# Kernel optimization log

Hardware: AMD Instinct MI355X
Metric: run time of the kernel (lower is better)

Reference implementation:

```python
import jax, jax.numpy as jnp
import numpy as np

N = 50000
E = 1600000
H = 64          # hidden_dim
EIN = 8         # edges_in_d (7 edge feats + 1 distance)
NORM_FACTOR = 100.0
NORM_CONSTANT = 1.0


def setup_inputs() -> dict:
    key = jax.random.key(0)
    ks = jax.random.split(key, 9)
    h = jax.random.normal(ks[0], (N, H), dtype=jnp.float32)
    coord = jax.random.normal(ks[1], (N, 3), dtype=jnp.float32)
    edge_index = jax.random.randint(ks[2], (2, E), 0, N)
    edge_attr = jax.random.normal(ks[3], (E, EIN), dtype=jnp.float32)
    # coord_mlp params: Linear(2H+EIN,H) -> SiLU -> Linear(H,H) -> SiLU -> Linear(H,1,bias=False)
    din = 2 * H + EIN
    W1 = jax.random.normal(ks[4], (din, H), dtype=jnp.float32) / np.sqrt(din)
    b1 = jnp.zeros((H,), dtype=jnp.float32)
    W2 = jax.random.normal(ks[5], (H, H), dtype=jnp.float32) / np.sqrt(H)
    b2 = jnp.zeros((H,), dtype=jnp.float32)
    # final layer xavier_uniform with gain=0.001 -> very small weights
    W3 = jax.random.uniform(ks[6], (H, 1), dtype=jnp.float32, minval=-1.0, maxval=1.0) * (0.001 * np.sqrt(6.0 / (H + 1)))
    return {"h": h, "coord": coord, "edge_index": edge_index, "edge_attr": edge_attr,
            "W1": W1, "b1": b1, "W2": W2, "b2": b2, "W3": W3}


def reference(h, coord, edge_index, edge_attr, W1, b1, W2, b2, W3):
    row, col = edge_index[0], edge_index[1]
    # coord2diff (norm_constant=1)
    coord_diff = coord[row] - coord[col]                       # [E,3]
    radial = jnp.sum(coord_diff ** 2, axis=1, keepdims=True)   # [E,1]
    norm = jnp.sqrt(radial + 1e-8)
    coord_diff = coord_diff / (norm + NORM_CONSTANT)
    # gather + concat -> edge MLP (SiLU activations), tanh=False path
    inp = jnp.concatenate([h[row], h[col], edge_attr], axis=1)  # [E, 2H+EIN]
    x1 = jax.nn.silu(inp @ W1 + b1)
    x2 = jax.nn.silu(x1 @ W2 + b2)
    scal = x2 @ W3                                              # [E,1]
    trans = coord_diff * scal                                   # [E,3]
    # unsorted_segment_sum with 'sum' aggregation -> divide by normalization_factor
    agg = jax.ops.segment_sum(trans, row, num_segments=N) / NORM_FACTOR  # [N,3]
    return coord + agg
```

## Files before the change

### kernel.cpp

```cpp
#include <hip/hip_runtime.h>
#include <math.h>

#define HD   64
#define EIN  8
#define SAS  168
#define W2S  72
#define NORM_INV 0.01f
#define NTH  256
#define NBLK 1280
#define NWAVES (NBLK * (NTH / 64))

typedef short bf16x8 __attribute__((ext_vector_type(8)));
typedef float f32x4  __attribute__((ext_vector_type(4)));
typedef float f4v    __attribute__((ext_vector_type(4)));

__device__ __forceinline__ unsigned short f2bf(float f) {
    union { float f; unsigned u; } v; v.f = f;
    unsigned r = v.u + 0x7FFFu + ((v.u >> 16) & 1u);
    return (unsigned short)(r >> 16);
}
__device__ __forceinline__ unsigned pk2(float a, float b) {
    return (unsigned)f2bf(a) | ((unsigned)f2bf(b) << 16);
}
__device__ __forceinline__ unsigned cvt_pk_bf16(float lo, float hi) {
    unsigned r;
    asm("v_cvt_pk_bf16_f32 %0, %1, %2" : "=v"(r) : "v"(lo), "v"(hi));
    return r;
}
__device__ __forceinline__ float silu_f(float x) {
    return x * __builtin_amdgcn_rcpf(1.0f + __expf(-x));
}
__device__ __forceinline__ bf16x8 pack_f8(f4v a, f4v b) {
    union { bf16x8 v; uint4 u; } pk;
    pk.u.x = pk2(a.x, a.y); pk.u.y = pk2(a.z, a.w);
    pk.u.z = pk2(b.x, b.y); pk.u.w = pk2(b.z, b.w);
    return pk.v;
}

__global__ void prep_h_kernel(const float* __restrict__ h, unsigned char* __restrict__ hf8,
                              int nq, const float* __restrict__ coord,
                              float* __restrict__ out, int n3) {
    int i = blockIdx.x * blockDim.x + threadIdx.x;
    if (i < nq) {
        f4v v = reinterpret_cast<const f4v*>(h)[i];
        int p = __builtin_amdgcn_cvt_pk_fp8_f32(v.x, v.y, 0, false);
        p     = __builtin_amdgcn_cvt_pk_fp8_f32(v.z, v.w, p, true);
        reinterpret_cast<int*>(hf8)[i] = p;
    }
    if (i < n3) out[i] = coord[i];
}

__global__ void prep_out_kernel(const float* __restrict__ coord,
                                float* __restrict__ out, int n3) {
    int i = blockIdx.x * blockDim.x + threadIdx.x;
    if (i < n3) out[i] = coord[i];
}

template <bool HB>
__global__ __launch_bounds__(NTH, 5) void egnn_mfma_kernel(
    const float* __restrict__ h,
    const unsigned char* __restrict__ hf8,
    const float* __restrict__ coord,
    const int*   __restrict__ eidx,
    const float* __restrict__ eattr,
    const float* __restrict__ W1f,
    const float* __restrict__ W2f,
    const float* __restrict__ b1,
    const float* __restrict__ b2,
    const float* __restrict__ W3,
    float* __restrict__ out,
    int E_)
{
    constexpr int LDS_BYTES = HB ? 28416 : 40704;
    __shared__ __align__(16) char lds[LDS_BYTES];

    unsigned long*  sW1f8 = (unsigned long*)lds;
    unsigned short* sW1b  = (unsigned short*)(lds + 8192);
    unsigned short* sW1   = (unsigned short*)lds;
    unsigned short* sW2   = (unsigned short*)(lds + (HB ? 9216  : 21504));
    unsigned short* sX1   = (unsigned short*)(lds + (HB ? 18432 : 30720));
    float*          sB1   = (float*)(lds + (HB ? 27648 : 39936));
    float*          sB2   = sB1 + 64;
    float*          sW3   = sB1 + 128;

    const int t = threadIdx.x;

    if (HB) {
        for (int f = t; f < 16 * 64; f += NTH) {
            int frag = f >> 6, ln = f & 63;
            int nt = frag >> 2, s = frag & 3;
            int mm = ln & 15, qq = ln >> 4;
            int n2 = nt * 16 + mm, kb = s * 32 + qq * 8;
            unsigned long v = 0;
#pragma unroll
            for (int j = 0; j < 8; j += 2) {
                float a = W1f[(kb + j) * 64 + n2] * 8.0f;
                float b = W1f[(kb + j + 1) * 64 + n2] * 8.0f;
                int p = __builtin_amdgcn_cvt_pk_fp8_f32(a, b, 0, false);
                v |= ((unsigned long)(unsigned)(p & 0xFFFF)) << (j * 8);
            }
            sW1f8[f] = v;
        }
        for (int i = t; i < 64 * 8; i += NTH) {
            int n2 = i >> 3, kk = i & 7;
            sW1b[i] = f2bf(W1f[(128 + kk) * 64 + n2]);
        }
    } else {
        for (int i = t; i < 136 * 64; i += NTH) {
            int k = i >> 6, n = i & 63;
            sW1[n * SAS + k] = f2bf(W1f[i]);
        }
        for (int i = t; i < 24 * 64; i += NTH) {
            int n = i / 24, k = 136 + (i - n * 24);
            sW1[n * SAS + k] = 0;
        }
    }
    for (int i = t; i < 64 * 64; i += NTH) {
        int k = i >> 6, n = i & 63;
        sW2[n * W2S + k] = f2bf(W2f[i]);
    }
    if (t < 64) sB1[t] = b1[t];
    else if (t < 128) sB2[t - 64] = b2[t - 64];
    else if (t < 192) sW3[t - 128] = W3[t - 128];
    __syncthreads();

    const int w = t >> 6, lane = t & 63;
    const int m = lane & 15, q = lane >> 4;

    unsigned short* x1Row = sX1 + (16 * w + m) * W2S;

    const int ngroups = (E_ + 15) >> 4;
    for (int g = blockIdx.x * (NTH / 64) + w; g < ngroups; g += NWAVES) {
        int e = g * 16 + m;
        int ec = (e < E_) ? e : (E_ - 1);
        int row = __builtin_nontemporal_load(eidx + ec);
        int col = __builtin_nontemporal_load(eidx + (size_t)E_ + ec);

        float cr = 0.f, cc = 0.f;
        if (q < 3) { cr = coord[row * 3 + q]; cc = coord[col * 3 + q]; }

        bf16x8 bf4;
        {
            union { bf16x8 v; uint4 u; } pk;
            pk.u.x = 0; pk.u.y = 0; pk.u.z = 0; pk.u.w = 0;
            if (q == 0) {
                const f4v* ea = (const f4v*)(eattr + (size_t)ec * EIN);
                f4v a0 = __builtin_nontemporal_load(ea);
                f4v a1 = __builtin_nontemporal_load(ea + 1);
                pk.u.x = cvt_pk_bf16(a0.x, a0.y);
                pk.u.y = cvt_pk_bf16(a0.z, a0.w);
                pk.u.z = cvt_pk_bf16(a1.x, a1.y);
                pk.u.w = cvt_pk_bf16(a1.z, a1.w);
            }
            bf4 = pk.v;
        }

        f32x4 acc1[4] = {};

        if (HB) {
            const unsigned long* hr8 = (const unsigned long*)(hf8 + (size_t)row * HD);
            const unsigned long* hc8 = (const unsigned long*)(hf8 + (size_t)col * HD);
            long b0 = (long)hr8[q];
            long b1v = (long)hr8[4 + q];
            long b2v = (long)hc8[q];
            long b3v = (long)hc8[4 + q];
            __builtin_amdgcn_s_setprio(1);
#define L1F8(S, B)                                                            \
            _Pragma("unroll")                                                 \
            for (int nt = 0; nt < 4; ++nt) {                                  \
                long a8 = (long)sW1f8[((nt << 2) | (S)) * 64 + lane];         \
                acc1[nt] = __builtin_amdgcn_mfma_f32_16x16x32_fp8_fp8(a8, B, acc1[nt], 0, 0, 0); \
            }
            L1F8(0, b0)
            L1F8(1, b1v)
            L1F8(2, b2v)
            L1F8(3, b3v)
#undef L1F8
#pragma unroll
            for (int nt = 0; nt < 4; ++nt) {
                bf16x8 afb = *(const bf16x8*)(sW1b + (16 * nt + m) * 8);
                acc1[nt] = __builtin_amdgcn_mfma_f32_16x16x32_bf16(afb, bf4, acc1[nt], 0, 0, 0);
            }
            __builtin_amdgcn_s_setprio(0);
        } else {
            bf16x8 bf[5];
            const f4v* hr = (const f4v*)(h + (size_t)row * HD);
            const f4v* hc = (const f4v*)(h + (size_t)col * HD);
#pragma unroll
            for (int s = 0; s < 4; ++s) {
                const f4v* src = (s < 2) ? hr : hc;
                f4v a = src[(s & 1) * 8 + q * 2];
                f4v b = src[(s & 1) * 8 + q * 2 + 1];
                bf[s] = pack_f8(a, b);
            }
            bf[4] = bf4;
#pragma unroll
            for (int s = 0; s < 5; ++s) {
#pragma unroll
                for (int nt = 0; nt < 4; ++nt) {
                    bf16x8 afrag = *(const bf16x8*)(sW1 + (16 * nt + m) * SAS + s * 32 + q * 8);
                    acc1[nt] = __builtin_amdgcn_mfma_f32_16x16x32_bf16(afrag, bf[s], acc1[nt], 0, 0, 0);
                }
            }
        }

        const float sc = HB ? 0.125f : 1.0f;
#pragma unroll
        for (int nt = 0; nt < 4; ++nt) {
            float4 bb = *(const float4*)(&sB1[16 * nt + 4 * q]);
            uint2 o;
            o.x = cvt_pk_bf16(silu_f(fmaf(acc1[nt][0], sc, bb.x)),
                              silu_f(fmaf(acc1[nt][1], sc, bb.y)));
            o.y = cvt_pk_bf16(silu_f(fmaf(acc1[nt][2], sc, bb.z)),
                              silu_f(fmaf(acc1[nt][3], sc, bb.w)));
            *((uint2*)(x1Row + 16 * nt + 4 * q)) = o;
        }

        f32x4 acc2[4] = {};
        __builtin_amdgcn_s_setprio(1);
#pragma unroll
        for (int s = 0; s < 2; ++s) {
            bf16x8 bfrag = *(const bf16x8*)(x1Row + s * 32 + q * 8);
#pragma unroll
            for (int nt = 0; nt < 4; ++nt) {
                bf16x8 afrag = *(const bf16x8*)(sW2 + (16 * nt + m) * W2S + s * 32 + q * 8);
                acc2[nt] = __builtin_amdgcn_mfma_f32_16x16x32_bf16(afrag, bfrag, acc2[nt], 0, 0, 0);
            }
        }
        __builtin_amdgcn_s_setprio(0);

        float p = 0.f;
#pragma unroll
        for (int nt = 0; nt < 4; ++nt) {
            float4 b2v2 = *(const float4*)(&sB2[16 * nt + 4 * q]);
            float4 w3v  = *(const float4*)(&sW3[16 * nt + 4 * q]);
            p = fmaf(silu_f(acc2[nt][0] + b2v2.x), w3v.x, p);
            p = fmaf(silu_f(acc2[nt][1] + b2v2.y), w3v.y, p);
            p = fmaf(silu_f(acc2[nt][2] + b2v2.z), w3v.z, p);
            p = fmaf(silu_f(acc2[nt][3] + b2v2.w), w3v.w, p);
        }
        p += __shfl_xor(p, 16);
        p += __shfl_xor(p, 32);

        float cd = cr - cc;
        float r2 = cd * cd;
        r2 += __shfl_xor(r2, 16);
        r2 += __shfl_xor(r2, 32);
        if (e < E_ && q < 3) {
            float inv = __builtin_amdgcn_rcpf(sqrtf(r2 + 1e-8f) + 1.0f);
            atomicAdd(&out[row * 3 + q], cd * (p * NORM_INV * inv));
        }
    }
}

extern "C" void kernel_launch(void* const* d_in, const int* in_sizes, int n_in,
                              void* d_out, int out_size, void* d_ws, size_t ws_size,
                              hipStream_t stream) {
    const float* h         = (const float*)d_in[0];
    const float* coord     = (const float*)d_in[1];
    const int*   eidx      = (const int*)  d_in[2];
    const float* edge_attr = (const float*)d_in[3];
    const float* W1        = (const float*)d_in[4];
    const float* b1        = (const float*)d_in[5];
    const float* W2        = (const float*)d_in[6];
    const float* b2        = (const float*)d_in[7];
    const float* W3        = (const float*)d_in[8];
    float* out = (float*)d_out;

    int E_ = in_sizes[2] / 2;
    int n3 = out_size;
    int nf = in_sizes[0];

    if (ws_size >= (size_t)nf) {
        unsigned char* hf8 = (unsigned char*)d_ws;
        int nq = nf / 4;
        int pgrid = (nq > n3 ? nq : n3);
        hipLaunchKernelGGL(prep_h_kernel, dim3((pgrid + 255) / 256), dim3(256), 0, stream,
                           h, hf8, nq, coord, out, n3);
        hipLaunchKernelGGL((egnn_mfma_kernel<true>), dim3(NBLK), dim3(NTH), 0, stream,
                           h, hf8, coord, eidx, edge_attr, W1, W2, b1, b2, W3, out, E_);
    } else {
        hipLaunchKernelGGL(prep_out_kernel, dim3((n3 + 255) / 256), dim3(256), 0, stream,
                           coord, out, n3);
        hipLaunchKernelGGL((egnn_mfma_kernel<false>), dim3(NBLK), dim3(NTH), 0, stream,
                           h, (const unsigned char*)nullptr, coord, eidx, edge_attr,
                           W1, W2, b1, b2, W3, out, E_);
    }
}
```

Baseline: 218.3 us.

## Run second MLP layer in FP8 MFMA and share reciprocal across SiLU pairs

In the HB path, W2 is prepacked into FP8 MFMA fragments scaled by 8, and x1 activations are stored as FP8 in LDS. The second layer then uses the 16x16x32 fp8 MFMA, and the scale is undone before the bias. SiLU is computed in pairs with one reciprocal per two values, and the block count rises to 1536 because the smaller LDS footprint permits more resident blocks. The aim is to cut LDS traffic and footprint, MFMA cost and transcendental count, at the price of lower precision for the hidden activations. The paired reciprocal can also overflow when the exponentials are large.

```diff
diff --git a/kernel.cpp b/kernel.cpp
--- a/kernel.cpp
+++ b/kernel.cpp
@@ -5,9 +5,10 @@
 #define EIN  8
 #define SAS  168
 #define W2S  72
+#define X1BS 72
 #define NORM_INV 0.01f
 #define NTH  256
-#define NBLK 1280
+#define NBLK 1536
 #define NWAVES (NBLK * (NTH / 64))
 
 typedef short bf16x8 __attribute__((ext_vector_type(8)));
@@ -29,6 +30,13 @@
 }
 __device__ __forceinline__ float silu_f(float x) {
     return x * __builtin_amdgcn_rcpf(1.0f + __expf(-x));
+}
+__device__ __forceinline__ void silu2(float x, float y, float& sx, float& sy) {
+    float a = 1.0f + __expf(-x);
+    float b = 1.0f + __expf(-y);
+    float r = __builtin_amdgcn_rcpf(a * b);
+    sx = x * (b * r);
+    sy = y * (a * r);
 }
 __device__ __forceinline__ bf16x8 pack_f8(f4v a, f4v b) {
     union { bf16x8 v; uint4 u; } pk;
@@ -71,15 +79,17 @@
     float* __restrict__ out,
     int E_)
 {
-    constexpr int LDS_BYTES = HB ? 28416 : 40704;
+    constexpr int LDS_BYTES = HB ? 18688 : 40704;
     __shared__ __align__(16) char lds[LDS_BYTES];
 
     unsigned long*  sW1f8 = (unsigned long*)lds;
     unsigned short* sW1b  = (unsigned short*)(lds + 8192);
+    unsigned long*  sW2f8 = (unsigned long*)(lds + 9216);
+    unsigned char*  sX1b  = (unsigned char*)(lds + 13312);
     unsigned short* sW1   = (unsigned short*)lds;
-    unsigned short* sW2   = (unsigned short*)(lds + (HB ? 9216  : 21504));
-    unsigned short* sX1   = (unsigned short*)(lds + (HB ? 18432 : 30720));
-    float*          sB1   = (float*)(lds + (HB ? 27648 : 39936));
+    unsigned short* sW2   = (unsigned short*)(lds + 21504);
+    unsigned short* sX1   = (unsigned short*)(lds + 30720);
+    float*          sB1   = (float*)(lds + (HB ? 17920 : 39936));
     float*          sB2   = sB1 + 64;
     float*          sW3   = sB1 + 128;
 
@@ -105,6 +115,21 @@
             int n2 = i >> 3, kk = i & 7;
             sW1b[i] = f2bf(W1f[(128 + kk) * 64 + n2]);
         }
+        for (int f = t; f < 8 * 64; f += NTH) {
+            int frag = f >> 6, ln = f & 63;
+            int nt = frag >> 1, s = frag & 1;
+            int mm = ln & 15, qq = ln >> 4;
+            int n2 = nt * 16 + mm, kb = s * 32 + qq * 8;
+            unsigned long v = 0;
+#pragma unroll
+            for (int j = 0; j < 8; j += 2) {
+                float a = W2f[(kb + j) * 64 + n2] * 8.0f;
+                float b = W2f[(kb + j + 1) * 64 + n2] * 8.0f;
+                int p = __builtin_amdgcn_cvt_pk_fp8_f32(a, b, 0, false);
+                v |= ((unsigned long)(unsigned)(p & 0xFFFF)) << (j * 8);
+            }
+            sW2f8[f] = v;
+        }
     } else {
         for (int i = t; i < 136 * 64; i += NTH) {
             int k = i >> 6, n = i & 63;
@@ -114,10 +139,10 @@
             int n = i / 24, k = 136 + (i - n * 24);
             sW1[n * SAS + k] = 0;
         }
-    }
-    for (int i = t; i < 64 * 64; i += NTH) {
-        int k = i >> 6, n = i & 63;
-        sW2[n * W2S + k] = f2bf(W2f[i]);
+        for (int i = t; i < 64 * 64; i += NTH) {
+            int k = i >> 6, n = i & 63;
+            sW2[n * W2S + k] = f2bf(W2f[i]);
+        }
     }
     if (t < 64) sB1[t] = b1[t];
     else if (t < 128) sB2[t - 64] = b2[t - 64];
@@ -127,7 +152,8 @@
     const int w = t >> 6, lane = t & 63;
     const int m = lane & 15, q = lane >> 4;
 
-    unsigned short* x1Row = sX1 + (16 * w + m) * W2S;
+    unsigned char*  x1RowB = sX1b + (16 * w + m) * X1BS;
+    unsigned short* x1Row  = sX1 + (16 * w + m) * W2S;
 
     const int ngroups = (E_ + 15) >> 4;
     for (int g = blockIdx.x * (NTH / 64) + w; g < ngroups; g += NWAVES) {
@@ -208,36 +234,59 @@
 #pragma unroll
         for (int nt = 0; nt < 4; ++nt) {
             float4 bb = *(const float4*)(&sB1[16 * nt + 4 * q]);
-            uint2 o;
-            o.x = cvt_pk_bf16(silu_f(fmaf(acc1[nt][0], sc, bb.x)),
-                              silu_f(fmaf(acc1[nt][1], sc, bb.y)));
-            o.y = cvt_pk_bf16(silu_f(fmaf(acc1[nt][2], sc, bb.z)),
-                              silu_f(fmaf(acc1[nt][3], sc, bb.w)));
-            *((uint2*)(x1Row + 16 * nt + 4 * q)) = o;
+            float s0, s1, s2, s3;
+            silu2(fmaf(acc1[nt][0], sc, bb.x), fmaf(acc1[nt][1], sc, bb.y), s0, s1);
+            silu2(fmaf(acc1[nt][2], sc, bb.z), fmaf(acc1[nt][3], sc, bb.w), s2, s3);
+            if (HB) {
+                int p = __builtin_amdgcn_cvt_pk_fp8_f32(s0, s1, 0, false);
+                p     = __builtin_amdgcn_cvt_pk_fp8_f32(s2, s3, p, true);
+                *((unsigned*)(x1RowB + 16 * nt + 4 * q)) = (unsigned)p;
+            } else {
+                uint2 o;
+                o.x = cvt_pk_bf16(s0, s1);
+                o.y = cvt_pk_bf16(s2, s3);
+                *((uint2*)(x1Row + 16 * nt + 4 * q)) = o;
+            }
         }
 
         f32x4 acc2[4] = {};
         __builtin_amdgcn_s_setprio(1);
-#pragma unroll
-        for (int s = 0; s < 2; ++s) {
-            bf16x8 bfrag = *(const bf16x8*)(x1Row + s * 32 + q * 8);
-#pragma unroll
-            for (int nt = 0; nt < 4; ++nt) {
-                bf16x8 afrag = *(const bf16x8*)(sW2 + (16 * nt + m) * W2S + s * 32 + q * 8);
-                acc2[nt] = __builtin_amdgcn_mfma_f32_16x16x32_bf16(afrag, bfrag, acc2[nt], 0, 0, 0);
+        if (HB) {
+#pragma unroll
+            for (int s = 0; s < 2; ++s) {
+                long bfrag = *(const long*)(x1RowB + s * 32 + q * 8);
+#pragma unroll
+                for (int nt = 0; nt < 4; ++nt) {
+                    long a8 = (long)sW2f8[((nt << 1) | s) * 64 + lane];
+                    acc2[nt] = __builtin_amdgcn_mfma_f32_16x16x32_fp8_fp8(a8, bfrag, acc2[nt], 0, 0, 0);
+                }
+            }
+        } else {
+#pragma unroll
+            for (int s = 0; s < 2; ++s) {
+                bf16x8 bfrag = *(const bf16x8*)(x1Row + s * 32 + q * 8);
+#pragma unroll
+                for (int nt = 0; nt < 4; ++nt) {
+                    bf16x8 afrag = *(const bf16x8*)(sW2 + (16 * nt + m) * W2S + s * 32 + q * 8);
+                    acc2[nt] = __builtin_amdgcn_mfma_f32_16x16x32_bf16(afrag, bfrag, acc2[nt], 0, 0, 0);
+                }
             }
         }
         __builtin_amdgcn_s_setprio(0);
 
+        const float sc2 = HB ? 0.125f : 1.0f;
         float p = 0.f;
 #pragma unroll
         for (int nt = 0; nt < 4; ++nt) {
             float4 b2v2 = *(const float4*)(&sB2[16 * nt + 4 * q]);
             float4 w3v  = *(const float4*)(&sW3[16 * nt + 4 * q]);
-            p = fmaf(silu_f(acc2[nt][0] + b2v2.x), w3v.x, p);
-            p = fmaf(silu_f(acc2[nt][1] + b2v2.y), w3v.y, p);
-            p = fmaf(silu_f(acc2[nt][2] + b2v2.z), w3v.z, p);
-            p = fmaf(silu_f(acc2[nt][3] + b2v2.w), w3v.w, p);
+            float s0, s1, s2, s3;
+            silu2(fmaf(acc2[nt][0], sc2, b2v2.x), fmaf(acc2[nt][1], sc2, b2v2.y), s0, s1);
+            silu2(fmaf(acc2[nt][2], sc2, b2v2.z), fmaf(acc2[nt][3], sc2, b2v2.w), s2, s3);
+            p = fmaf(s0, w3v.x, p);
+            p = fmaf(s1, w3v.y, p);
+            p = fmaf(s2, w3v.z, p);
+            p = fmaf(s3, w3v.w, p);
         }
         p += __shfl_xor(p, 16);
         p += __shfl_xor(p, 32);
```

New measurement: 220.9 us. About the same (+1.2%).
